# Performance work log

Hardware: AMD Instinct MI355X
Metric: run time of the kernel (lower is better)

The kernel has to match this reference:

```python
import jax, jax.numpy as jnp
import numpy as np

EPS = 1e-8
MIN_VAL = -1e7  # module default min_val=-10000000.0


def _div_safe(n, d):
    return n / jnp.maximum(d, EPS)


def _cosine_pairwise(v1, v2):
    # v1: (B,L1,H), v2: (B,L2,H) -> (B,L1,L2)
    n1 = jnp.linalg.norm(v1, axis=2, keepdims=True)
    n2 = jnp.linalg.norm(v2, axis=2, keepdims=True)
    a = jnp.einsum('bik,bjk->bij', v1, v2)
    return _div_safe(a, n1 * jnp.swapaxes(n2, 1, 2))


def _masked_max(v, mask, axis, keepdims=False):
    rep = jnp.where(mask > 0, v, MIN_VAL)
    val = jnp.max(rep, axis=axis, keepdims=keepdims)
    m = jnp.max(jnp.broadcast_to(mask, v.shape), axis=axis, keepdims=keepdims)
    return val * m


def _masked_mean(v, mask, axis, keepdims=False):
    s = jnp.sum(v * mask, axis=axis, keepdims=keepdims)
    c = jnp.sum(jnp.broadcast_to(mask, v.shape), axis=axis, keepdims=keepdims)
    return _div_safe(s, c)


def _cos_sim(a, b, axis):
    # torch F.cosine_similarity semantics: dot / (max(|a|,eps)*max(|b|,eps))
    dot = jnp.sum(a * b, axis=axis)
    na = jnp.maximum(jnp.linalg.norm(a, axis=axis), EPS)
    nb = jnp.maximum(jnp.linalg.norm(b, axis=axis), EPS)
    return dot / (na * nb)


def _mpm(v1, v2, w):
    # v1, v2: (B,L,H); w: (P,H) -> ((B,L,1), (B,L,P))
    mv1 = _cos_sim(v1, v2, 2)[..., None]
    v1w = w[None, None] * v1[:, :, None, :]  # (B,L,P,H)
    v2w = w[None, None] * v2[:, :, None, :]
    return mv1, _cos_sim(v1w, v2w, 3)


def _mpm_pairwise(v1, v2, w):
    # v1: (B,L1,H), v2: (B,L2,H), w: (P,H) -> (B,L1,L2,P)
    v1w = w[None, :, None, :] * v1[:, None, :, :]  # (B,P,L1,H)
    v2w = w[None, :, None, :] * v2[:, None, :, :]  # (B,P,L2,H)
    n1 = jnp.linalg.norm(v1w, axis=3, keepdims=True)
    n2 = jnp.linalg.norm(v2w, axis=3, keepdims=True)
    n = jnp.einsum('bpik,bpjk->bpij', v1w, v2w)
    d = n1 * jnp.swapaxes(n2, 2, 3)
    return jnp.transpose(_div_safe(n, d), (0, 2, 3, 1))


def setup_inputs() -> dict:
    key = jax.random.key(0)
    ks = jax.random.split(key, 8)
    B, L, H, P = 32, 128, 100, 20
    return {
        'context_p': jax.random.normal(ks[0], (B, L, H), dtype=jnp.float32),
        'mask_p': jax.random.randint(ks[1], (B, L), 0, 2, dtype=jnp.int32),
        'context_h': jax.random.normal(ks[2], (B, L, H), dtype=jnp.float32),
        'mask_h': jax.random.randint(ks[3], (B, L), 0, 2, dtype=jnp.int32),
        'w0': jax.random.uniform(ks[4], (P, H), dtype=jnp.float32),
        'w1': jax.random.uniform(ks[5], (P, H), dtype=jnp.float32),
        'w2': jax.random.uniform(ks[6], (P, H), dtype=jnp.float32),
        'w3': jax.random.uniform(ks[7], (P, H), dtype=jnp.float32),
    }


def reference(context_p, mask_p, context_h, mask_h, w0, w1, w2, w3):
    mask_p = mask_p.astype(jnp.float32)
    mask_h = mask_h.astype(jnp.float32)
    B, Lp, H = context_p.shape
    Lh = context_h.shape[1]

    mask_p_h = mask_p[:, :, None] * mask_h[:, None, :]   # (B,Lp,Lh)
    mask_h_p = jnp.swapaxes(mask_p_h, 1, 2)              # (B,Lh,Lp)
    cp = context_p * mask_p[..., None]
    ch = context_h * mask_h[..., None]

    # --- pairwise cosine + masked max/mean pooling ---
    cos = _cosine_pairwise(cp, ch)                        # (B,Lp,Lh)
    cosT = jnp.swapaxes(cos, 1, 2)
    cos_max_p = _masked_max(cos, mask_p_h, 2, True)
    cos_mean_p = _masked_mean(cos, mask_p_h, 2, True)
    cos_max_h = _masked_max(cosT, mask_h_p, 2, True)
    cos_mean_h = _masked_mean(cosT, mask_h_p, 2, True)

    # --- full match (is_forward=True: last real token) ---
    idx_p = jnp.clip(jnp.sum(mask_p, 1).astype(jnp.int32) - 1, 0)[:, None, None]
    idx_h = jnp.clip(jnp.sum(mask_h, 1).astype(jnp.int32) - 1, 0)[:, None, None]
    cp_last = jnp.take_along_axis(cp, jnp.broadcast_to(idx_p, (B, 1, H)), axis=1)
    ch_last = jnp.take_along_axis(ch, jnp.broadcast_to(idx_h, (B, 1, H)), axis=1)
    mv_p_f1, mv_p_fP = _mpm(cp, jnp.broadcast_to(ch_last, (B, Lp, H)), w0)
    mv_h_f1, mv_h_fP = _mpm(ch, jnp.broadcast_to(cp_last, (B, Lh, H)), w0)

    # --- maxpool match ---
    mv_max = _mpm_pairwise(cp, ch, w1)                    # (B,Lp,Lh,P)
    mv_p_max = _masked_max(mv_max, mask_p_h[..., None], 2)
    mv_p_mean = _masked_mean(mv_max, mask_p_h[..., None], 2)
    mv_maxT = jnp.transpose(mv_max, (0, 2, 1, 3))
    mv_h_max = _masked_max(mv_maxT, mask_h_p[..., None], 2)
    mv_h_mean = _masked_mean(mv_maxT, mask_h_p[..., None], 2)

    # --- attentive match (mean) ---
    att_mean_h = _div_safe(jnp.einsum('bij,bjh->bih', cos, ch),
                           jnp.sum(cos, 2, keepdims=True))
    att_mean_p = _div_safe(jnp.einsum('bij,bih->bjh', cos, cp),
                           jnp.swapaxes(jnp.sum(cos, 1, keepdims=True), 1, 2))
    mv_p_am1, mv_p_amP = _mpm(cp, att_mean_h, w2)
    mv_h_am1, mv_h_amP = _mpm(ch, att_mean_p, w2)

    # --- max-attentive match ---
    att_h = ch[:, None, :, :] * cos[:, :, :, None]        # (B,Lp,Lh,H)
    att_p_t = cp[:, None, :, :] * cosT[:, :, :, None]     # (B,Lh,Lp,H) == att_p.permute(0,2,1,3)
    att_max_h = _masked_max(att_h, mask_p_h[..., None], 2)
    att_max_p = _masked_max(att_p_t, mask_h_p[..., None], 2)
    mv_p_ax1, mv_p_axP = _mpm(cp, att_max_h, w3)
    mv_h_ax1, mv_h_axP = _mpm(ch, att_max_p, w3)

    mv_p = jnp.concatenate([cos_max_p, cos_mean_p, mv_p_f1, mv_p_fP,
                            mv_p_max, mv_p_mean, mv_p_am1, mv_p_amP,
                            mv_p_ax1, mv_p_axP], axis=2)
    mv_h = jnp.concatenate([cos_max_h, cos_mean_h, mv_h_f1, mv_h_fP,
                            mv_h_max, mv_h_mean, mv_h_am1, mv_h_amP,
                            mv_h_ax1, mv_h_axP], axis=2)
    return mv_p, mv_h
```

## Files before the change

kernel.cpp:

```cpp
#include <hip/hip_runtime.h>
#include <math.h>


namespace {
constexpr int B = 32;
constexpr int L = 128;
constexpr int H = 100;
constexpr int P = 20;
constexpr int C = 105;
constexpr int TI = 8;
constexpr int SMEM_BYTES = 50176;
constexpr float EPSF = 1e-8f;
constexpr float MINV = -1e7f;
}

typedef unsigned short u16;
typedef unsigned int u32;
typedef short sh8 __attribute__((ext_vector_type(8)));
typedef float f4 __attribute__((ext_vector_type(4)));

__device__ __forceinline__ u16 f2bf(float f) {
    u32 u = __float_as_uint(f);
    u += 0x7FFFu + ((u >> 16) & 1u);
    return (u16)(u >> 16);
}
__device__ __forceinline__ float bf2f(u32 h) {
    return __uint_as_float(h << 16);
}

__global__ void k_prep(const float* __restrict__ ctx_p, const int* __restrict__ mask_p,
                       const float* __restrict__ ctx_h, const int* __restrict__ mask_h,
                       const float* __restrict__ w1,
                       float* __restrict__ cp, float* __restrict__ ch,
                       u16* __restrict__ cpb, u16* __restrict__ chb,
                       float* __restrict__ np_, float* __restrict__ nh_,
                       float* __restrict__ nwp, float* __restrict__ nwh)
{
    const int b = blockIdx.y, i = blockIdx.x, side = blockIdx.z, t = threadIdx.x;
    const float* ctx = side ? ctx_h : ctx_p;
    const int*  mask = side ? mask_h : mask_p;
    float* dst  = side ? ch  : cp;
    u16*   dstb = side ? chb : cpb;
    float* nrm  = side ? nh_ : np_;
    float* nw   = side ? nwh : nwp;

    const int row = b * L + i;
    __shared__ __align__(16) float sv2[H];
    const float m = (float)mask[row];
    float v = 0.f;
    if (t < H) {
        v = ctx[row * H + t] * m;
        dst[row * H + t] = v;
        sv2[t] = v * v;
    }
    dstb[row * 128 + t] = f2bf(v);
    __syncthreads();

    const int w = t >> 6, ln = t & 63;
    int g = -1, seg = 0;
    if (w == 0) { if (ln < 60) { g = ln / 5; seg = ln % 5; } }
    else        { if (ln < 45) { g = 12 + ln / 5; seg = ln % 5; } }
    if (g >= 0) {
        const float4* v4 = (const float4*)sv2;
        float acc = 0.f;
        if (g < P) {
            const float4* w4 = (const float4*)(w1 + g * H);
            #pragma unroll
            for (int k = seg * 5; k < seg * 5 + 5; ++k) {
                float4 wv_ = w4[k], s = v4[k];
                acc += wv_.x * wv_.x * s.x + wv_.y * wv_.y * s.y +
                       wv_.z * wv_.z * s.z + wv_.w * wv_.w * s.w;
            }
        } else {
            #pragma unroll
            for (int k = seg * 5; k < seg * 5 + 5; ++k) {
                float4 s = v4[k];
                acc += s.x + s.y + s.z + s.w;
            }
        }
        float a1 = __shfl(acc, ln + 1), a2 = __shfl(acc, ln + 2);
        float a3 = __shfl(acc, ln + 3), a4 = __shfl(acc, ln + 4);
        if (seg == 0) {
            float s = acc + a1 + a2 + a3 + a4;
            if (g < P) nw[row * P + g] = sqrtf(s);
            else       nrm[row] = sqrtf(s);
        }
    }
}

__global__ __launch_bounds__(512) void
k_main(const float* __restrict__ cp, const float* __restrict__ ch,
       const u16* __restrict__ cpb, const u16* __restrict__ chb,
       const float* __restrict__ np_, const float* __restrict__ nh_,
       const float* __restrict__ nw1p, const float* __restrict__ nw1h,
       const int* __restrict__ mask_p, const int* __restrict__ mask_h,
       const float* __restrict__ w0, const float* __restrict__ w1,
       const float* __restrict__ w2, const float* __restrict__ w3,
       float* __restrict__ out)
{
    __shared__ __align__(16) char smem[SMEM_BYTES];
    const int bx = blockIdx.x, b = blockIdx.y, t = threadIdx.x;
    const int wv = t >> 6, ln = t & 63;
    float* out_p = out;
    float* out_h = out + (size_t)B * L * C;

    if (bx < P) {
        const int p = bx;
        u16*  sB    = (u16*)smem;
        float* snwA = (float*)(smem + 34816);
        float* snwB = (float*)(smem + 35328);
        float* smA  = (float*)(smem + 35840);
        float* smB  = (float*)(smem + 36352);
        float* pJmax= (float*)(smem + 36864);
        float* pJsum= (float*)(smem + 37376);
        float* pImax= (float*)(smem + 37888);
        float* pIsum= (float*)(smem + 41984);
        float* sRed = (float*)(smem + 46080);

        if (t < 128) {
            snwA[t] = nw1p[(b * L + t) * P + p];
            snwB[t] = nw1h[(b * L + t) * P + p];
            smA[t] = (float)mask_p[b * L + t];
            smB[t] = (float)mask_h[b * L + t];
        }
        __syncthreads();

        if (t < 64) {
            float a0 = smB[t], a1 = smB[t + 64];
            float mx = fmaxf(a0, a1), sm = a0 + a1;
            for (int d = 1; d < 64; d <<= 1) {
                mx = fmaxf(mx, __shfl_xor(mx, d));
                sm += __shfl_xor(sm, d);
            }
            if (t == 0) { sRed[2] = mx; sRed[3] = sm; }
        } else if (t < 128) {
            const int l = t - 64;
            float a0 = smA[l], a1 = smA[l + 64];
            float mx = fmaxf(a0, a1), sm = a0 + a1;
            for (int d = 1; d < 64; d <<= 1) {
                mx = fmaxf(mx, __shfl_xor(mx, d));
                sm += __shfl_xor(sm, d);
            }
            if (l == 0) { sRed[0] = mx; sRed[1] = sm; }
        }

        {
            const uint4* src = (const uint4*)(chb + (size_t)b * L * 128);
            #pragma unroll
            for (int it = 0; it < 4; ++it) {
                int idx = it * 512 + t;
                int row = idx >> 4, kc = (idx & 15) * 8;
                uint4 v = src[idx];
                *(uint4*)&sB[row * 136 + kc] = v;
            }
        }
        __syncthreads();

        const int m = ln & 15, q = ln >> 4;

        float swv[4][8];
        #pragma unroll
        for (int ks = 0; ks < 4; ++ks)
            #pragma unroll
            for (int e = 0; e < 8; ++e) {
                int k = ks * 32 + q * 8 + e;
                float w = (k < H) ? w1[p * H + k] : 0.f;
                swv[ks][e] = w * w;
            }

        f4 acc[8];
        #pragma unroll
        for (int ct = 0; ct < 8; ++ct) acc[ct] = (f4){0.f, 0.f, 0.f, 0.f};

        const uint4* gA = (const uint4*)(cpb + (size_t)(b * L + wv * 16 + m) * 128);

        #pragma unroll
        for (int ks = 0; ks < 4; ++ks) {
            uint4 va = gA[ks * 4 + q];
            sh8 af;
            {
                u32 vs[4] = {va.x, va.y, va.z, va.w};
                u32 r[4];
                #pragma unroll
                for (int e = 0; e < 4; ++e) {
                    float f0 = bf2f(vs[e] & 0xffffu) * swv[ks][2 * e];
                    float f1 = bf2f(vs[e] >> 16) * swv[ks][2 * e + 1];
                    r[e] = (u32)f2bf(f0) | ((u32)f2bf(f1) << 16);
                }
                uint4 o = {r[0], r[1], r[2], r[3]};
                af = __builtin_bit_cast(sh8, o);
            }
            const int ko = ks * 32 + q * 8;
            #pragma unroll
            for (int ct = 0; ct < 8; ++ct) {
                sh8 bb = *(const sh8*)&sB[(ct * 16 + m) * 136 + ko];
                acc[ct] = __builtin_amdgcn_mfma_f32_16x16x32_bf16(af, bb, acc[ct], 0, 0, 0);
            }
        }

        float nB[8], mBv[8], imax[8], isum[8];
        #pragma unroll
        for (int ct = 0; ct < 8; ++ct) {
            const int j = ct * 16 + m;
            nB[ct] = snwB[j]; mBv[ct] = smB[j];
            imax[ct] = MINV; isum[ct] = 0.f;
        }
        #pragma unroll
        for (int reg = 0; reg < 4; ++reg) {
            const int i = wv * 16 + q * 4 + reg;
            const float na = snwA[i];
            const float ma = smA[i];
            float jmax = MINV, jsum = 0.f;
            #pragma unroll
            for (int ct = 0; ct < 8; ++ct) {
                float v = acc[ct][reg] *
                          __builtin_amdgcn_rcpf(fmaxf(na * nB[ct], EPSF));
                jmax = fmaxf(jmax, mBv[ct] > 0.f ? v : MINV);
                jsum += mBv[ct] > 0.f ? v : 0.f;
                imax[ct] = fmaxf(imax[ct], ma > 0.f ? v : MINV);
                isum[ct] += ma > 0.f ? v : 0.f;
            }
            for (int d = 1; d < 16; d <<= 1) {
                jmax = fmaxf(jmax, __shfl_xor(jmax, d));
                jsum += __shfl_xor(jsum, d);
            }
            if (m == 0) { pJmax[i] = jmax; pJsum[i] = jsum; }
        }
        #pragma unroll
        for (int ct = 0; ct < 8; ++ct) {
            float mx = imax[ct], sm = isum[ct];
            mx = fmaxf(mx, __shfl_xor(mx, 16)); sm += __shfl_xor(sm, 16);
            mx = fmaxf(mx, __shfl_xor(mx, 32)); sm += __shfl_xor(sm, 32);
            if (q == 0) { const int j = ct * 16 + m; pImax[wv * 128 + j] = mx; pIsum[wv * 128 + j] = sm; }
        }
        __syncthreads();

        if (t < 128) {
            const int i = t;
            const float ma = smA[i];
            const float mm = ma * sRed[2];
            const float cnt = ma * sRed[3];
            float* orow = out_p + ((size_t)b * L + i) * C;
            orow[23 + p] = pJmax[i] * mm;
            orow[43 + p] = ma * pJsum[i] / fmaxf(cnt, EPSF);

            const float mb = smB[i];
            float hmax = MINV, hsum = 0.f;
            #pragma unroll
            for (int s = 0; s < 8; ++s) {
                hmax = fmaxf(hmax, pImax[s * 128 + i]);
                hsum += pIsum[s * 128 + i];
            }
            float* hrow = out_h + ((size_t)b * L + i) * C;
            hrow[23 + p] = hmax * mb * sRed[0];
            hrow[43 + p] = mb * hsum / fmaxf(mb * sRed[1], EPSF);
        }
    } else {
        const int e = bx - P;
        const int side = e >> 4, tile = e & 15;
        const int i0 = tile * TI;
        const float* A   = side ? ch : cp;
        const float* Bv  = side ? cp : ch;
        const u16*  Ab16 = side ? chb : cpb;
        const u16*  Bvb  = side ? cpb : chb;
        const float* nA_ = side ? nh_ : np_;
        const float* nB_ = side ? np_ : nh_;
        const int* maskA = side ? mask_h : mask_p;
        const int* maskB = side ? mask_p : mask_h;
        float* outBase = out + ((size_t)side * B * L + (size_t)b * L) * C;

        float* scosC = (float*)(smem + 34816);
        float* sa    = (float*)(smem + 38912);
        float* sam   = (float*)(smem + 42112);
        float* sax   = (float*)(smem + 45312);
        float* sl    = (float*)(smem + 48512);
        float* snB   = (float*)(smem + 48912);
        u16*  cidx  = (u16*)(smem + 49424);
        float* snA   = (float*)(smem + 49680);
        int*   pnv   = (int*)(smem + 49712);

        if (wv == 0) {
            int m0 = maskB[b * L + ln], m1 = maskB[b * L + 64 + ln];
            unsigned long long b0 = __ballot(m0 > 0);
            unsigned long long b1 = __ballot(m1 > 0);
            unsigned long long pre = (1ull << ln) - 1ull;
            int n0 = __popcll(b0);
            if (m0 > 0) cidx[__popcll(b0 & pre)] = (u16)ln;
            if (m1 > 0) cidx[n0 + __popcll(b1 & pre)] = (u16)(64 + ln);
            if (ln == 0) *pnv = n0 + __popcll(b1);
        } else if (wv >= 2) {
            for (int x = t - 128; x < TI * 128; x += 384) {
                int il = x >> 7, k = x & 127;
                if (k < H) sa[il * 100 + k] = A[((size_t)b * L + i0 + il) * H + k];
            }
        }
        __syncthreads();
        const int nv = *pnv;
        const int nct = (nv + 15) >> 4;

        {
            const uint4* src = (const uint4*)(Bvb + (size_t)b * L * 128);
            for (int c = t; c < nct * 256; c += 512) {
                int jj = c >> 4, cc = c & 15;
                uint4 v;
                if (jj < nv) v = src[(int)cidx[jj] * 16 + cc];
                else { v.x = v.y = v.z = v.w = 0u; }
                *(uint4*)(smem + jj * 272 + cc * 16) = v;
            }
            if (t < 128) snB[t] = (t < nv) ? nB_[b * L + (int)cidx[t]] : 0.f;
            else if (t < 136) snA[t - 128] = nA_[b * L + i0 + (t - 128)];
            if (wv == 1) {
                int last = nv - 1; if (last < 0) last = 0;
                const float* lr = Bv + ((size_t)b * L + last) * H;
                sl[ln] = lr[ln];
                if (ln + 64 < H) sl[ln + 64] = lr[ln + 64];
            }
        }
        __syncthreads();

        const int m = ln & 15, q = ln >> 4;
        if (wv < nct) {
            const uint4* gA = (const uint4*)(Ab16 + (size_t)(b * L + i0 + (m & 7)) * 128);
            f4 acc0 = (f4){0.f, 0.f, 0.f, 0.f};
            #pragma unroll
            for (int ks = 0; ks < 4; ++ks) {
                uint4 va = gA[ks * 4 + q];
                if (m >= 8) { va.x = va.y = va.z = va.w = 0u; }
                sh8 af = __builtin_bit_cast(sh8, va);
                const int ko2 = (ks * 32 + q * 8) * 2;
                sh8 bb = *(const sh8*)(smem + (wv * 16 + m) * 272 + ko2);
                acc0 = __builtin_amdgcn_mfma_f32_16x16x32_bf16(af, bb, acc0, 0, 0, 0);
            }
            if (q < 2) {
                #pragma unroll
                for (int reg = 0; reg < 4; ++reg) {
                    const int i = q * 4 + reg;
                    const int jj = wv * 16 + m;
                    scosC[i * 128 + jj] = acc0[reg] *
                        __builtin_amdgcn_rcpf(fmaxf(snA[i] * snB[jj], EPSF));
                }
            }
        }
        __syncthreads();

        {
            const int il = wv;
            const int gi = i0 + il;
            if (ln < 50) {
                const float mA = (float)maskA[b * L + gi];
                float am0 = 0.f, am1 = 0.f, ax0 = MINV, ax1 = MINV;
                float scj = 0.f, cmx = MINV;
                const u32* bp = (const u32*)smem + ln;
                const float* cr = scosC + il * 128;
                #pragma unroll 4
                for (int jj = 0; jj < nv; ++jj) {
                    u32 pk = bp[jj * 68];
                    float cj = cr[jj];
                    scj += cj; cmx = fmaxf(cmx, cj);
                    float v0 = cj * __uint_as_float(pk << 16);
                    float v1 = cj * __uint_as_float(pk & 0xffff0000u);
                    am0 += v0; am1 += v1;
                    ax0 = fmaxf(ax0, v0); ax1 = fmaxf(ax1, v1);
                }
                const float rs = __builtin_amdgcn_rcpf(fmaxf(scj, EPSF));
                const float mm = (nv > 0) ? mA : 0.f;
                sam[il * 100 + 2 * ln] = am0 * rs; sam[il * 100 + 2 * ln + 1] = am1 * rs;
                sax[il * 100 + 2 * ln] = ax0 * mm; sax[il * 100 + 2 * ln + 1] = ax1 * mm;
                if (ln == 0) {
                    float* orow = outBase + (size_t)gi * C;
                    orow[0] = cmx * mm;
                    orow[1] = mA * scj / fmaxf(mA * (float)nv, EPSF);
                }
            }
        }
        __syncthreads();

        for (int task = t; task < TI * 63; task += 512) {
            const int il = task / 63, c = task - il * 63;
            float* orow = outBase + (size_t)(i0 + il) * C;
            const float4* a4 = (const float4*)(sa + il * 100);
            if (c < 60) {
                const int grp = c / 20, p = c - grp * 20;
                const float* wrow = (grp == 0 ? w0 : grp == 1 ? w2 : w3) + p * H;
                const float* oth = grp == 0 ? sl : (grp == 1 ? sam : sax) + il * 100;
                const float4* w4 = (const float4*)wrow;
                const float4* o4 = (const float4*)oth;
                float d = 0.f, na = 0.f, nb = 0.f;
                #pragma unroll 5
                for (int k = 0; k < H / 4; ++k) {
                    float4 w = w4[k], a = a4[k], o = o4[k];
                    float ww;
                    ww = w.x * w.x; d += ww * a.x * o.x; na += ww * a.x * a.x; nb += ww * o.x * o.x;
                    ww = w.y * w.y; d += ww * a.y * o.y; na += ww * a.y * a.y; nb += ww * o.y * o.y;
                    ww = w.z * w.z; d += ww * a.z * o.z; na += ww * a.z * a.z; nb += ww * o.z * o.z;
                    ww = w.w * w.w; d += ww * a.w * o.w; na += ww * a.w * a.w; nb += ww * o.w * o.w;
                }
                const int base = (grp == 0) ? 3 : (grp == 1) ? 64 : 85;
                orow[base + p] = d / (fmaxf(sqrtf(na), EPSF) * fmaxf(sqrtf(nb), EPSF));
            } else {
                const float* oth = (c == 60) ? sl : ((c == 61) ? sam : sax) + il * 100;
                const float4* o4 = (const float4*)oth;
                float d = 0.f, na = 0.f, nb = 0.f;
                #pragma unroll 5
                for (int k = 0; k < H / 4; ++k) {
                    float4 a = a4[k], o = o4[k];
                    d += a.x * o.x + a.y * o.y + a.z * o.z + a.w * o.w;
                    na += a.x * a.x + a.y * a.y + a.z * a.z + a.w * a.w;
                    nb += o.x * o.x + o.y * o.y + o.z * o.z + o.w * o.w;
                }
                orow[(c == 60) ? 2 : (c == 61) ? 63 : 84] =
                    d / (fmaxf(sqrtf(na), EPSF) * fmaxf(sqrtf(nb), EPSF));
            }
        }
    }
}

extern "C" void kernel_launch(void* const* d_in, const int* in_sizes, int n_in,
                              void* d_out, int out_size, void* d_ws, size_t ws_size,
                              hipStream_t stream)
{
    const float* ctx_p = (const float*)d_in[0];
    const int*   mask_p = (const int*)d_in[1];
    const float* ctx_h = (const float*)d_in[2];
    const int*   mask_h = (const int*)d_in[3];
    const float* w0 = (const float*)d_in[4];
    const float* w1 = (const float*)d_in[5];
    const float* w2 = (const float*)d_in[6];
    const float* w3 = (const float*)d_in[7];
    float* out = (float*)d_out;

    float* ws   = (float*)d_ws;
    float* cp   = ws;
    float* ch   = cp   + B * L * H;
    float* np_  = ch   + B * L * H;
    float* nh_  = np_  + B * L;
    float* nw1p = nh_  + B * L;
    float* nw1h = nw1p + B * L * P;
    u16*   cpb  = (u16*)(nw1h + B * L * P);
    u16*   chb  = cpb + B * L * 128;

    k_prep<<<dim3(L, B, 2), dim3(128), 0, stream>>>(
        ctx_p, mask_p, ctx_h, mask_h, w1,
        cp, ch, cpb, chb, np_, nh_, nw1p, nw1h);
    k_main<<<dim3(P + 32, B), dim3(512), 0, stream>>>(
        cp, ch, cpb, chb, np_, nh_, nw1p, nw1h, mask_p, mask_h,
        w0, w1, w2, w3, out);
}
```

Baseline: 124.7 us.

## Compute weighted multi-perspective cosine dot products with bf16 MFMA

Replaces the per-thread scalar loops for the weighted cosine matches (dot products and norms for 60 perspectives plus the unweighted ones) with a small bf16 MFMA GEMM. Elementwise products of context and attention vectors are packed into bf16 tiles in shared memory, the squared weights form the other operand, and the results are staged in shared memory before the final normalisation. It also moves the cosine sum/max reductions to wave shuffles over the full row, taking them out of the attentive loop. This adds bf16 rounding to the products and norms, which risks accuracy, plus extra shared-memory passes and syncs.

```diff
diff --git a/kernel.cpp b/kernel.cpp
--- a/kernel.cpp
+++ b/kernel.cpp
@@ -26,6 +26,9 @@
 }
 __device__ __forceinline__ float bf2f(u32 h) {
     return __uint_as_float(h << 16);
+}
+__device__ __forceinline__ u32 pack2(float a, float b) {
+    return (u32)f2bf(a) | ((u32)f2bf(b) << 16);
 }
 
 __global__ void k_prep(const float* __restrict__ ctx_p, const int* __restrict__ mask_p,
@@ -271,14 +274,16 @@
 
         float* scosC = (float*)(smem + 34816);
         float* sa    = (float*)(smem + 38912);
-        float* sam   = (float*)(smem + 42112);
-        float* sax   = (float*)(smem + 45312);
-        float* sl    = (float*)(smem + 48512);
-        float* snB   = (float*)(smem + 48912);
-        u16*  cidx  = (u16*)(smem + 49424);
-        float* snA   = (float*)(smem + 49680);
-        int*   pnv   = (int*)(smem + 49712);
-
+        float* sam   = (float*)(smem + 42496);
+        float* sax   = (float*)(smem + 46080);
+        float* sl    = (float*)(smem + 49664);
+        float* snB   = (float*)(smem + 42496);
+        float* snA   = (float*)(smem + 43008);
+        u16*  cidx  = (u16*)(smem + 43040);
+        int*   pnv   = (int*)(smem + 50112);
+
+        scosC[t] = 0.f;
+        scosC[t + 512] = 0.f;
         if (wv == 0) {
             int m0 = maskB[b * L + ln], m1 = maskB[b * L + 64 + ln];
             unsigned long long b0 = __ballot(m0 > 0);
@@ -291,7 +296,7 @@
         } else if (wv >= 2) {
             for (int x = t - 128; x < TI * 128; x += 384) {
                 int il = x >> 7, k = x & 127;
-                if (k < H) sa[il * 100 + k] = A[((size_t)b * L + i0 + il) * H + k];
+                if (k < H) sa[il * 112 + k] = A[((size_t)b * L + i0 + il) * H + k];
             }
         }
         __syncthreads();
@@ -346,71 +351,133 @@
         {
             const int il = wv;
             const int gi = i0 + il;
+            const float mA = (float)maskA[b * L + gi];
+            float c0 = scosC[il * 128 + ln], c1 = scosC[il * 128 + 64 + ln];
+            float scj = c0 + c1;
+            float mv0 = (ln < nv) ? c0 : MINV;
+            float mv1 = (ln + 64 < nv) ? c1 : MINV;
+            float cmx = fmaxf(mv0, mv1);
+            for (int d = 1; d < 64; d <<= 1) {
+                scj += __shfl_xor(scj, d);
+                cmx = fmaxf(cmx, __shfl_xor(cmx, d));
+            }
+            const float mm = (nv > 0) ? mA : 0.f;
+            if (ln == 0) {
+                float* orow = outBase + (size_t)gi * C;
+                orow[0] = cmx * mm;
+                orow[1] = mA * scj / fmaxf(mA * (float)nv, EPSF);
+            }
             if (ln < 50) {
-                const float mA = (float)maskA[b * L + gi];
                 float am0 = 0.f, am1 = 0.f, ax0 = MINV, ax1 = MINV;
-                float scj = 0.f, cmx = MINV;
                 const u32* bp = (const u32*)smem + ln;
                 const float* cr = scosC + il * 128;
                 #pragma unroll 4
                 for (int jj = 0; jj < nv; ++jj) {
                     u32 pk = bp[jj * 68];
                     float cj = cr[jj];
-                    scj += cj; cmx = fmaxf(cmx, cj);
                     float v0 = cj * __uint_as_float(pk << 16);
                     float v1 = cj * __uint_as_float(pk & 0xffff0000u);
                     am0 += v0; am1 += v1;
                     ax0 = fmaxf(ax0, v0); ax1 = fmaxf(ax1, v1);
                 }
                 const float rs = __builtin_amdgcn_rcpf(fmaxf(scj, EPSF));
-                const float mm = (nv > 0) ? mA : 0.f;
-                sam[il * 100 + 2 * ln] = am0 * rs; sam[il * 100 + 2 * ln + 1] = am1 * rs;
-                sax[il * 100 + 2 * ln] = ax0 * mm; sax[il * 100 + 2 * ln + 1] = ax1 * mm;
-                if (ln == 0) {
-                    float* orow = outBase + (size_t)gi * C;
-                    orow[0] = cmx * mm;
-                    orow[1] = mA * scj / fmaxf(mA * (float)nv, EPSF);
+                sam[il * 112 + 2 * ln] = am0 * rs; sam[il * 112 + 2 * ln + 1] = am1 * rs;
+                sax[il * 112 + 2 * ln] = ax0 * mm; sax[il * 112 + 2 * ln + 1] = ax1 * mm;
+            }
+        }
+        __syncthreads();
+
+        for (int idx = t; idx < 8 * 8 * 17; idx += 512) {
+            int kc = (idx % 17) * 8;
+            int tmp = idx / 17;
+            int il = tmp >> 3, col = tmp & 7;
+            const float* sa_il  = sa  + il * 112;
+            const float* sam_il = sam + il * 112;
+            const float* sax_il = sax + il * 112;
+            const float* p1 = (col >= 4) ? (col == 4 ? sl : col == 5 ? sam_il : sax_il)
+                                         : sa_il;
+            const float* p2 = (col == 0 || col == 4) ? sl :
+                              (col == 1 || col == 5) ? sam_il :
+                              (col == 2 || col == 6) ? sax_il : sa_il;
+            u32 ow[4];
+            #pragma unroll
+            for (int e2 = 0; e2 < 4; ++e2) {
+                int k0 = kc + 2 * e2;
+                float f0 = (col < 7 && k0 < H)     ? p1[k0] * p2[k0]         : 0.f;
+                float f1 = (col < 7 && k0 + 1 < H) ? p1[k0 + 1] * p2[k0 + 1] : 0.f;
+                ow[e2] = pack2(f0, f1);
+            }
+            uint4 o = {ow[0], ow[1], ow[2], ow[3]};
+            *(uint4*)(smem + (tmp * 136 + kc) * 2) = o;
+        }
+        for (int idx = t; idx < 64 * 17; idx += 512) {
+            int kc = (idx % 17) * 8;
+            int row = idx / 17;
+            u32 ow[4];
+            #pragma unroll
+            for (int e2 = 0; e2 < 4; ++e2) {
+                int k0 = kc + 2 * e2;
+                float f0 = 0.f, f1 = 0.f;
+                if (row < 60) {
+                    const float* wr = (row < 20) ? w0 + row * H :
+                                      (row < 40) ? w2 + (row - 20) * H :
+                                                   w3 + (row - 40) * H;
+                    if (k0 < H)     { float w = wr[k0];     f0 = w * w; }
+                    if (k0 + 1 < H) { float w = wr[k0 + 1]; f1 = w * w; }
+                } else if (row == 60) {
+                    f0 = (k0 < H) ? 1.f : 0.f;
+                    f1 = (k0 + 1 < H) ? 1.f : 0.f;
                 }
-            }
+                ow[e2] = pack2(f0, f1);
+            }
+            uint4 o = {ow[0], ow[1], ow[2], ow[3]};
+            *(uint4*)(smem + 17408 + (row * 136 + kc) * 2) = o;
+        }
+        __syncthreads();
+
+        f4 d3[4];
+        #pragma unroll
+        for (int Mt = 0; Mt < 4; ++Mt) d3[Mt] = (f4){0.f, 0.f, 0.f, 0.f};
+        {
+            const int cn = m & 7;
+            #pragma unroll
+            for (int ks = 0; ks < 4; ++ks) {
+                const int ko2 = (ks * 32 + q * 8) * 2;
+                sh8 bb = *(const sh8*)(smem + ((wv * 8 + cn) * 136) * 2 + ko2);
+                #pragma unroll
+                for (int Mt = 0; Mt < 4; ++Mt) {
+                    sh8 aa = *(const sh8*)(smem + 17408 + ((Mt * 16 + m) * 136) * 2 + ko2);
+                    d3[Mt] = __builtin_amdgcn_mfma_f32_16x16x32_bf16(aa, bb, d3[Mt], 0, 0, 0);
+                }
+            }
+        }
+        __syncthreads();
+
+        if (m < 8) {
+            #pragma unroll
+            for (int Mt = 0; Mt < 4; ++Mt)
+                #pragma unroll
+                for (int reg = 0; reg < 4; ++reg)
+                    ((float*)smem)[wv * 512 + (Mt * 16 + q * 4 + reg) * 8 + m] = d3[Mt][reg];
         }
         __syncthreads();
 
         for (int task = t; task < TI * 63; task += 512) {
             const int il = task / 63, c = task - il * 63;
-            float* orow = outBase + (size_t)(i0 + il) * C;
-            const float4* a4 = (const float4*)(sa + il * 100);
+            int row, dcol, nbcol, chn;
             if (c < 60) {
-                const int grp = c / 20, p = c - grp * 20;
-                const float* wrow = (grp == 0 ? w0 : grp == 1 ? w2 : w3) + p * H;
-                const float* oth = grp == 0 ? sl : (grp == 1 ? sam : sax) + il * 100;
-                const float4* w4 = (const float4*)wrow;
-                const float4* o4 = (const float4*)oth;
-                float d = 0.f, na = 0.f, nb = 0.f;
-                #pragma unroll 5
-                for (int k = 0; k < H / 4; ++k) {
-                    float4 w = w4[k], a = a4[k], o = o4[k];
-                    float ww;
-                    ww = w.x * w.x; d += ww * a.x * o.x; na += ww * a.x * a.x; nb += ww * o.x * o.x;
-                    ww = w.y * w.y; d += ww * a.y * o.y; na += ww * a.y * a.y; nb += ww * o.y * o.y;
-                    ww = w.z * w.z; d += ww * a.z * o.z; na += ww * a.z * a.z; nb += ww * o.z * o.z;
-                    ww = w.w * w.w; d += ww * a.w * o.w; na += ww * a.w * a.w; nb += ww * o.w * o.w;
-                }
-                const int base = (grp == 0) ? 3 : (grp == 1) ? 64 : 85;
-                orow[base + p] = d / (fmaxf(sqrtf(na), EPSF) * fmaxf(sqrtf(nb), EPSF));
+                const int grp = c / 20;
+                row = c; dcol = grp; nbcol = 4 + grp;
+                chn = ((grp == 0) ? 3 : (grp == 1) ? 64 : 85) + (c - grp * 20);
             } else {
-                const float* oth = (c == 60) ? sl : ((c == 61) ? sam : sax) + il * 100;
-                const float4* o4 = (const float4*)oth;
-                float d = 0.f, na = 0.f, nb = 0.f;
-                #pragma unroll 5
-                for (int k = 0; k < H / 4; ++k) {
-                    float4 a = a4[k], o = o4[k];
-                    d += a.x * o.x + a.y * o.y + a.z * o.z + a.w * o.w;
-                    na += a.x * a.x + a.y * a.y + a.z * a.z + a.w * a.w;
-                    nb += o.x * o.x + o.y * o.y + o.z * o.z + o.w * o.w;
-                }
-                orow[(c == 60) ? 2 : (c == 61) ? 63 : 84] =
-                    d / (fmaxf(sqrtf(na), EPSF) * fmaxf(sqrtf(nb), EPSF));
-            }
+                const int cc = c - 60;
+                row = 60; dcol = cc; nbcol = 4 + cc;
+                chn = (cc == 0) ? 2 : (cc == 1) ? 63 : 84;
+            }
+            const float* Dr = (const float*)smem + il * 512 + row * 8;
+            float d = Dr[dcol], na = Dr[3], nb = Dr[nbcol];
+            outBase[(size_t)(i0 + il) * C + chn] =
+                d / (fmaxf(sqrtf(na), EPSF) * fmaxf(sqrtf(nb), EPSF));
         }
     }
 }
```

Result: no change. 124.0 us (-0.5%).
